# Kernel tuning notes

Measured on AMD Instinct MI355X. Metric: run time of the kernel, lower is better.

The kernel has to match this reference:

```python
import jax, jax.numpy as jnp
import numpy as np

N = 50000      # nodes
E = 1600000    # edges (before self loops)
IN = 128       # in_channels
HID = 64       # hidden_channels
HEADS = 2
NEG_SLOPE = 0.2  # PyG GATConv default


def setup_inputs() -> dict:
    key = jax.random.key(0)
    ks = jax.random.split(key, 12)
    s = 0.05
    return {
        "x": jax.random.normal(ks[0], (N, IN), jnp.float32),
        "edge_index": jax.random.randint(ks[1], (2, E), 0, N, dtype=jnp.int32),
        # layer 1: GATConv(IN -> HID, heads=HEADS, concat=True)
        "W1": jax.random.normal(ks[2], (IN, HEADS * HID), jnp.float32) * s,
        "a_src1": jax.random.normal(ks[3], (HEADS, HID), jnp.float32) * s,
        "a_dst1": jax.random.normal(ks[4], (HEADS, HID), jnp.float32) * s,
        "b1": jax.random.normal(ks[5], (HEADS * HID,), jnp.float32) * s,
        # layer 2: GATConv(HEADS*HID -> HID, heads=1, concat=False)
        "W2": jax.random.normal(ks[6], (HEADS * HID, HID), jnp.float32) * s,
        "a_src2": jax.random.normal(ks[7], (1, HID), jnp.float32) * s,
        "a_dst2": jax.random.normal(ks[8], (1, HID), jnp.float32) * s,
        "b2": jax.random.normal(ks[9], (HID,), jnp.float32) * s,
        "lin_w": jax.random.normal(ks[10], (HID, 1), jnp.float32) * s,
        "lin_b": jax.random.normal(ks[11], (1,), jnp.float32) * s,
    }


def gat_layer(x, src, dst, W, a_src, a_dst, b, heads, out_ch, concat, n):
    # linear transform: [n, heads, out_ch]
    h = (x @ W).reshape(n, heads, out_ch)
    # per-node attention logit halves  [n, heads]
    al_src = jnp.sum(h * a_src, axis=-1)
    al_dst = jnp.sum(h * a_dst, axis=-1)
    # per-edge logits (gather) + LeakyReLU  [e, heads]
    e = jax.nn.leaky_relu(al_src[src] + al_dst[dst], negative_slope=NEG_SLOPE)
    # segment softmax over edges grouped by destination node
    m = jax.ops.segment_max(e, dst, num_segments=n)
    ex = jnp.exp(e - m[dst])
    denom = jax.ops.segment_sum(ex, dst, num_segments=n)
    alpha = ex / (denom[dst] + 1e-16)
    # weighted message scatter-add  [n, heads, out_ch]
    out = jax.ops.segment_sum(h[src] * alpha[:, :, None], dst, num_segments=n)
    out = out.reshape(n, heads * out_ch) if concat else out.mean(axis=1)
    return out + b


def reference(x, edge_index, W1, a_src1, a_dst1, b1, W2, a_src2, a_dst2, b2, lin_w, lin_b):
    # PyG GATConv adds self loops by default
    loops = jnp.arange(N, dtype=edge_index.dtype)
    src = jnp.concatenate([edge_index[0], loops])
    dst = jnp.concatenate([edge_index[1], loops])
    h = gat_layer(x, src, dst, W1, a_src1, a_dst1, b1, HEADS, HID, True, N)
    h = jax.nn.elu(h)
    h = gat_layer(h, src, dst, W2, a_src2, a_dst2, b2, 1, HID, False, N)
    return (h @ lin_w + lin_b)[:, 0]  # squeeze(-1) -> [N]
```

## Files before the change

kernel.cpp:

```cpp
#include <hip/hip_runtime.h>
#include <hip/hip_fp16.h>


#define LEAKY(x) ((x) > 0.f ? (x) : 0.2f * (x))

typedef float v2f __attribute__((ext_vector_type(2)));
typedef _Float16 f16x8 __attribute__((ext_vector_type(8)));
typedef __fp16 h16x2 __attribute__((ext_vector_type(2)));
typedef float f32x4 __attribute__((ext_vector_type(4)));


template <int VPT>
__global__ __launch_bounds__(256) void bucket_cnt_kernel(const int* __restrict__ ei, int E, int n,
                                                         int* __restrict__ bc) {
  __shared__ int lc[256];
  int t = threadIdx.x;
  lc[t] = 0;
  __syncthreads();
  int base = blockIdx.x * (256 * VPT) + t;
  int tot = E + n;
#pragma unroll
  for (int u = 0; u < VPT; ++u) {
    int i = base + u * 256;
    if (i < tot) {
      int d = (i < E) ? ei[E + i] : (i - E);
      atomicAdd(&lc[d >> 8], 1);
    }
  }
  __syncthreads();
  if (lc[t]) atomicAdd(&bc[t], lc[t]);
}

template <int VPT>
__global__ __launch_bounds__(256) void bucket_scatter_kernel(const int* __restrict__ ei, int E,
                                                             int n,
                                                             const int* __restrict__ bcnt,
                                                             int* __restrict__ bcur_rel,
                                                             unsigned* __restrict__ entries,
                                                             int B) {
  __shared__ int lc[256];
  __shared__ int lbase[256];
  __shared__ int bscan[256];
  int t = threadIdx.x;
  lc[t] = 0;
  int v = (t < B) ? bcnt[t] : 0;
  bscan[t] = v;
  __syncthreads();
  for (int s = 1; s < 256; s <<= 1) {
    int a = (t >= s) ? bscan[t - s] : 0;
    __syncthreads();
    bscan[t] += a;
    __syncthreads();
  }
  int excl = bscan[t] - v;

  int base = blockIdx.x * (256 * VPT) + t;
  int tot = E + n;
  int bb[VPT], ll[VPT];
  unsigned pk[VPT];
#pragma unroll
  for (int u = 0; u < VPT; ++u) {
    int i = base + u * 256;
    bb[u] = -1;
    if (i < tot) {
      int s, d;
      if (i < E) { s = ei[i]; d = ei[E + i]; }
      else       { s = d = i - E; }
      int b = d >> 8;
      bb[u] = b;
      ll[u] = atomicAdd(&lc[b], 1);
      pk[u] = (unsigned)s | ((unsigned)(d & 255) << 16);
    }
  }
  __syncthreads();
  if (lc[t]) lbase[t] = excl + atomicAdd(&bcur_rel[t], lc[t]);
  __syncthreads();
#pragma unroll
  for (int u = 0; u < VPT; ++u)
    if (bb[u] >= 0) entries[lbase[bb[u]] + ll[u]] = pk[u];
}

__global__ __launch_bounds__(256) void csr_build_kernel(const unsigned* __restrict__ entries,
                                                        const int* __restrict__ bcnt,
                                                        int* __restrict__ off,
                                                        unsigned short* __restrict__ eps,
                                                        int n, int B) {
  __shared__ int bscan[256];
  __shared__ int hist[256];
  __shared__ int scn[256];
  __shared__ int cur[256];
  int b = blockIdx.x, t = threadIdx.x;
  int v = (t < B) ? bcnt[t] : 0;
  bscan[t] = v;
  __syncthreads();
  for (int s = 1; s < 256; s <<= 1) {
    int a = (t >= s) ? bscan[t - s] : 0;
    __syncthreads();
    bscan[t] += a;
    __syncthreads();
  }
  int k0 = (b == 0) ? 0 : bscan[b - 1];
  int k1 = bscan[b];
  __syncthreads();

  hist[t] = 0;
  __syncthreads();
  for (int k = k0 + t; k < k1; k += 256) atomicAdd(&hist[(entries[k] >> 16) & 255], 1);
  __syncthreads();
  int hv = hist[t];
  scn[t] = hv;
  __syncthreads();
  for (int s = 1; s < 256; s <<= 1) {
    int a = (t >= s) ? scn[t - s] : 0;
    __syncthreads();
    scn[t] += a;
    __syncthreads();
  }
  int excl = scn[t] - hv;
  int d = (b << 8) + t;
  if (d < n) off[d] = k0 + excl;
  cur[t] = k0 + excl;
  __syncthreads();
  for (int k = k0 + t; k < k1; k += 256) {
    unsigned e = entries[k];
    unsigned dl = (e >> 16) & 255;
    int p = atomicAdd(&cur[dl], 1);
    eps[p] = (unsigned short)(e & 0xffffu);
  }
}


__global__ __launch_bounds__(256) void wprep_kernel(const float* __restrict__ W1,
                                                    const float* __restrict__ W2,
                                                    const float* __restrict__ as2,
                                                    const float* __restrict__ ad2,
                                                    const float* __restrict__ lw,
                                                    unsigned short* __restrict__ Wp1,
                                                    float* __restrict__ vsrc2,
                                                    float* __restrict__ vdst2,
                                                    float* __restrict__ vlin,
                                                    int* __restrict__ bcnt,
                                                    int* __restrict__ bcur_rel,
                                                    int* __restrict__ off,
                                                    int B, int n, int Etot) {
  if (blockIdx.x == 0) {
    if (threadIdx.x <= (unsigned)B) {
      bcnt[threadIdx.x] = 0;
      bcur_rel[threadIdx.x] = 0;
    }
    if (threadIdx.x == 255) off[n] = Etot;
  }
  int t = blockIdx.x * 256 + threadIdx.x;
  if (t < 16384) {
    int e = t;
    int i = e & 7;
    int c = (e >> 3) & 15;
    int g = (e >> 7) & 3;
    int kk = (e >> 9) & 3;
    int cn = e >> 11;
    int k = kk * 32 + g * 8 + i;
    int col = cn * 16 + c;
    __half h = __float2half(W1[k * 128 + col]);
    Wp1[e] = *(unsigned short*)&h;
  } else if (t < 16384 + 128) {
    int k = t - 16384;
    float a = 0.f, b = 0.f, s = 0.f;
    for (int cc = 0; cc < 64; ++cc) {
      float w = W2[k * 64 + cc];
      a = fmaf(w, as2[cc], a);
      b = fmaf(w, ad2[cc], b);
      s = fmaf(w, lw[cc], s);
    }
    vsrc2[k] = a;
    vdst2[k] = b;
    vlin[k] = s;
  }
}


__global__ __launch_bounds__(256) void gemm1_kernel(const float* __restrict__ X,
                                                    const uint4* __restrict__ Wp,
                                                    const float* __restrict__ a_src,
                                                    const float* __restrict__ a_dst,
                                                    unsigned char* __restrict__ Hout,
                                                    float2* __restrict__ als,
                                                    float2* __restrict__ ald, int n) {
  __shared__ float Xl[32 * 132];
  __shared__ float lgt[2][2][2][16];
  int t = threadIdx.x;
  int wave = t >> 6, lane = t & 63;
  int wm = wave >> 1, wn = wave & 1;
  int g = lane >> 4, c = lane & 15;
  int nb0 = blockIdx.x * 32;

  {
    const float4* Xg = (const float4*)X;
    float4* Xs = (float4*)Xl;
#pragma unroll
    for (int u = 0; u < 4; ++u) {
      int idx = u * 256 + t;
      int r = idx >> 5, c4 = idx & 31;
      int row = nb0 + r;
      int rc = row < n ? row : (n - 1);
      Xs[r * 33 + c4] = Xg[(size_t)rc * 32 + c4];
    }
  }
  __syncthreads();

  f16x8 af[4];
  const float* xr = Xl + (wm * 16 + c) * 132 + g * 8;
#pragma unroll
  for (int kk = 0; kk < 4; ++kk) {
    float4 x0 = *(const float4*)(xr + kk * 32);
    float4 x1 = *(const float4*)(xr + kk * 32 + 4);
    union { f16x8 v; h16x2 p[4]; } A;
    A.p[0] = __builtin_amdgcn_cvt_pkrtz(x0.x, x0.y);
    A.p[1] = __builtin_amdgcn_cvt_pkrtz(x0.z, x0.w);
    A.p[2] = __builtin_amdgcn_cvt_pkrtz(x1.x, x1.y);
    A.p[3] = __builtin_amdgcn_cvt_pkrtz(x1.z, x1.w);
    af[kk] = A.v;
  }

  f32x4 acc[4];
  f32x4 z = {0.f, 0.f, 0.f, 0.f};
#pragma unroll
  for (int cn = 0; cn < 4; ++cn) acc[cn] = z;
#pragma unroll
  for (int cn = 0; cn < 4; ++cn) {
    int cng = wn * 4 + cn;
#pragma unroll
    for (int kk = 0; kk < 4; ++kk) {
      union { uint4 u; f16x8 v; } B;
      B.u = Wp[(cng * 4 + kk) * 64 + lane];
      acc[cn] = __builtin_amdgcn_mfma_f32_16x16x32_f16(af[kk], B.v, acc[cn], 0, 0, 0);
    }
  }

  float asv[4], adv[4];
#pragma unroll
  for (int cn = 0; cn < 4; ++cn) {
    int col_l = wn * 64 + cn * 16 + c;
    asv[cn] = a_src[col_l];
    adv[cn] = a_dst[col_l];
  }
  float ps[4] = {0.f, 0.f, 0.f, 0.f};
  float pd[4] = {0.f, 0.f, 0.f, 0.f};
#pragma unroll
  for (int cn = 0; cn < 4; ++cn) {
#pragma unroll
    for (int r = 0; r < 4; ++r) {
      float v = acc[cn][r];
      ps[r] = fmaf(v, asv[cn], ps[r]);
      pd[r] = fmaf(v, adv[cn], pd[r]);
      int noder = nb0 + wm * 16 + g * 4 + r;
      int colg = wn * 64 + cn * 16 + c;
      if (noder < n) {
        int b8 = __builtin_amdgcn_cvt_pk_fp8_f32(v, v, 0, false);
        Hout[(size_t)noder * 128 + colg] = (unsigned char)(b8 & 0xff);
      }
    }
  }
#pragma unroll
  for (int r = 0; r < 4; ++r) {
#pragma unroll
    for (int m = 1; m <= 8; m <<= 1) {
      ps[r] += __shfl_xor(ps[r], m, 64);
      pd[r] += __shfl_xor(pd[r], m, 64);
    }
  }
  if (c == 0) {
#pragma unroll
    for (int r = 0; r < 4; ++r) {
      lgt[wm][wn][0][g * 4 + r] = ps[r];
      lgt[wm][wn][1][g * 4 + r] = pd[r];
    }
  }
  __syncthreads();
  if (t < 32) {
    int wmm = t >> 4, row = t & 15;
    int node = nb0 + wmm * 16 + row;
    if (node < n) {
      als[node] = make_float2(lgt[wmm][0][0][row], lgt[wmm][1][0][row]);
      ald[node] = make_float2(lgt[wmm][0][1][row], lgt[wmm][1][1][row]);
    }
  }
}


__global__ __launch_bounds__(256) void agg1_kernel(const unsigned char* __restrict__ Hb8,
                                                   const float2* __restrict__ als,
                                                   const float2* __restrict__ ald,
                                                   const unsigned short* __restrict__ eps,
                                                   const int* __restrict__ off,
                                                   const float* __restrict__ b1,
                                                   const float* __restrict__ vsrc2,
                                                   const float* __restrict__ vdst2,
                                                   const float* __restrict__ vlin,
                                                   float2* __restrict__ gsrc,
                                                   float* __restrict__ adst2, int n) {
  __shared__ float wlds[4][128];
  int wid = (blockIdx.x * 256 + threadIdx.x) >> 6;
  int lane = threadIdx.x & 63;
  if (wid >= n) return;
  wid = __builtin_amdgcn_readfirstlane(wid);
  int wslot = (threadIdx.x >> 6) & 3;
  int half = lane >> 5;
  int k0 = off[wid], k1 = off[wid + 1];
  const unsigned short* Hu = (const unsigned short*)Hb8;
  float2 advv = ald[wid];
  float* wrow = &wlds[wslot][half << 6];

  float ax = 0.f, ay = 0.f, den = 0.f;

  for (int kb = k0; kb < k1; kb += 64) {
    int rem = min(k1 - kb, 64);
    int e = kb + (lane < rem ? lane : rem - 1);
    unsigned pp = eps[e];
    float2 l = als[pp];
    float g0 = __expf(LEAKY(l.x + advv.x));
    float g1 = __expf(LEAKY(l.y + advv.y));
    wlds[wslot][lane] = g0;
    wlds[wslot][64 + lane] = g1;

#define EDGE1(jj)                                                                   \
  {                                                                                 \
    unsigned p = (unsigned)__builtin_amdgcn_readlane((int)pp, (jj));                \
    float w = wrow[(jj)];                                                           \
    unsigned short hv = Hu[(p << 6) | (unsigned)lane];                              \
    v2f hf = __builtin_amdgcn_cvt_pk_f32_fp8((int)hv, false);                       \
    den += w;                                                                       \
    ax = fmaf(hf.x, w, ax);                                                         \
    ay = fmaf(hf.y, w, ay);                                                         \
  }

    int nb = rem >> 3;
    for (int b = 0; b < nb; ++b) {
      int jb = b << 3;
#pragma unroll
      for (int j = 0; j < 8; ++j) EDGE1(jb + j);
    }
    for (int jj = nb << 3; jj < rem; ++jj) EDGE1(jj);
#undef EDGE1
  }

  float inv = 1.f / (den + 1e-16f);
  float2 bv = ((const float2*)b1)[lane];
  float r0 = ax * inv + bv.x;
  float r1 = ay * inv + bv.y;
  r0 = r0 > 0.f ? r0 : (__expf(r0) - 1.f);
  r1 = r1 > 0.f ? r1 : (__expf(r1) - 1.f);
  float2 vs = ((const float2*)vsrc2)[lane];
  float2 vd = ((const float2*)vdst2)[lane];
  float2 vl = ((const float2*)vlin)[lane];
  float ps = r0 * vs.x + r1 * vs.y;
  float pd = r0 * vd.x + r1 * vd.y;
  float sv = r0 * vl.x + r1 * vl.y;
#pragma unroll
  for (int m = 1; m <= 32; m <<= 1) {
    ps += __shfl_xor(ps, m, 64);
    pd += __shfl_xor(pd, m, 64);
    sv += __shfl_xor(sv, m, 64);
  }
  if (lane == 0) {
    gsrc[wid] = make_float2(ps, sv);
    adst2[wid] = pd;
  }
}

__global__ __launch_bounds__(256) void agg2_kernel(const float2* __restrict__ gsrc,
                                                   const float* __restrict__ adst2,
                                                   const unsigned short* __restrict__ eps,
                                                   const int* __restrict__ off,
                                                   const float* __restrict__ b2,
                                                   const float* __restrict__ lin_w,
                                                   const float* __restrict__ lin_b,
                                                   float* __restrict__ out, int n) {
  int wid = (blockIdx.x * 256 + threadIdx.x) >> 6;
  int lane = threadIdx.x & 63;
  if (wid >= n) return;
  wid = __builtin_amdgcn_readfirstlane(wid);
  int k0 = off[wid], k1 = off[wid + 1];
  float adv = adst2[wid];

  float num = 0.f, den = 0.f;
  for (int kb = k0; kb < k1; kb += 64) {
    int e = kb + lane;
    bool ok = e < k1;
    unsigned pp = eps[ok ? e : k0];
    float2 g = gsrc[pp];
    float w = ok ? __expf(LEAKY(g.x + adv)) : 0.f;
    num = fmaf(w, g.y, num);
    den += w;
  }
  float bt = b2[lane] * lin_w[lane];
#pragma unroll
  for (int m = 1; m <= 32; m <<= 1) {
    num += __shfl_xor(num, m, 64);
    den += __shfl_xor(den, m, 64);
    bt  += __shfl_xor(bt, m, 64);
  }
  if (lane == 0) out[wid] = num / (den + 1e-16f) + bt + lin_b[0];
}


static inline size_t alignup(size_t v) { return (v + 255) & ~(size_t)255; }

extern "C" void kernel_launch(void* const* d_in, const int* in_sizes, int n_in,
                              void* d_out, int out_size, void* d_ws, size_t ws_size,
                              hipStream_t stream) {
  const float* x   = (const float*)d_in[0];
  const int*   ei  = (const int*)d_in[1];
  const float* W1  = (const float*)d_in[2];
  const float* as1 = (const float*)d_in[3];
  const float* ad1 = (const float*)d_in[4];
  const float* b1  = (const float*)d_in[5];
  const float* W2  = (const float*)d_in[6];
  const float* as2 = (const float*)d_in[7];
  const float* ad2 = (const float*)d_in[8];
  const float* b2  = (const float*)d_in[9];
  const float* lw  = (const float*)d_in[10];
  const float* lb  = (const float*)d_in[11];
  float* out = (float*)d_out;

  const int N = out_size;
  const int E = in_sizes[1] / 2;
  const int Etot = E + N;
  const int B = (N + 255) >> 8;

  char* p = (char*)d_ws;
  int* bcnt = (int*)p;  p += alignup((size_t)(B + 1) * 4);
  int* bcur_rel = (int*)p; p += alignup((size_t)(B + 1) * 4);
  unsigned* entries = (unsigned*)p; p += alignup((size_t)Etot * 4);
  int* off  = (int*)p;  p += alignup((size_t)(N + 1) * 4);
  unsigned short* eps = (unsigned short*)p; p += alignup((size_t)Etot * 2);
  float2* als = (float2*)p; p += alignup((size_t)N * 8);
  float2* ald = (float2*)p; p += alignup((size_t)N * 8);
  float2* gsrc = (float2*)p; p += alignup((size_t)N * 8);
  float* adst2 = (float*)p; p += alignup((size_t)N * 4);
  unsigned char* h1b = (unsigned char*)p; p += alignup((size_t)N * 128);
  unsigned short* wp1 = (unsigned short*)p; p += alignup((size_t)16384 * 2);
  float* vsrc2 = (float*)p; p += alignup((size_t)128 * 4);
  float* vdst2 = (float*)p; p += alignup((size_t)128 * 4);
  float* vlin  = (float*)p; p += alignup((size_t)128 * 4);

  constexpr int VPT = 8;
  int egrid = (Etot + 256 * VPT - 1) / (256 * VPT);

  wprep_kernel<<<65, 256, 0, stream>>>(W1, W2, as2, ad2, lw, wp1, vsrc2, vdst2, vlin,
                                       bcnt, bcur_rel, off, B, N, Etot);
  bucket_cnt_kernel<VPT><<<egrid, 256, 0, stream>>>(ei, E, N, bcnt);
  bucket_scatter_kernel<VPT><<<egrid, 256, 0, stream>>>(ei, E, N, bcnt, bcur_rel,
                                                        entries, B);
  csr_build_kernel<<<B, 256, 0, stream>>>(entries, bcnt, off, eps, N, B);

  gemm1_kernel<<<(N + 31) / 32, 256, 0, stream>>>(
      x, (const uint4*)wp1, as1, ad1, h1b, als, ald, N);
  agg1_kernel<<<(N + 3) / 4, 256, 0, stream>>>(h1b, als, ald, eps, off, b1,
                                               vsrc2, vdst2, vlin, gsrc, adst2, N);
  agg2_kernel<<<(N + 3) / 4, 256, 0, stream>>>(gsrc, adst2, eps, off, b2, lw, lb, out, N);
}
```

Measured before the change: 145.9 us.

## Merge weight prep with bucket count and GEMM with bucket scatter launches

Independent stages are now horizontally fused into shared launches: the weight preparation runs in the same grid as the bucket counting, and the layer-1 GEMM blocks share a grid with the bucket scatter blocks. Zeroing moves into its own tiny kernel, and the CSR build kernel goes from 256 to 512 threads per block. The aim is fewer launch gaps and letting the compute-bound GEMM overlap the atomic-heavy scatter. The cost is an extra launch and larger shared-memory use per combined block, which may lower occupancy.

```diff
diff --git a/kernel.cpp b/kernel.cpp
--- a/kernel.cpp
+++ b/kernel.cpp
@@ -10,14 +10,63 @@
 typedef float f32x4 __attribute__((ext_vector_type(4)));
 
 
+__global__ __launch_bounds__(256) void zero_kernel(int* __restrict__ bcnt,
+                                                   int* __restrict__ bcur_rel,
+                                                   int* __restrict__ off,
+                                                   int B, int n, int Etot) {
+  if (threadIdx.x <= (unsigned)B) {
+    bcnt[threadIdx.x] = 0;
+    bcur_rel[threadIdx.x] = 0;
+  }
+  if (threadIdx.x == 255) off[n] = Etot;
+}
+
+
 template <int VPT>
-__global__ __launch_bounds__(256) void bucket_cnt_kernel(const int* __restrict__ ei, int E, int n,
-                                                         int* __restrict__ bc) {
+__global__ __launch_bounds__(256) void prep_cnt_kernel(const float* __restrict__ W1,
+                                                       const float* __restrict__ W2,
+                                                       const float* __restrict__ as2,
+                                                       const float* __restrict__ ad2,
+                                                       const float* __restrict__ lw,
+                                                       unsigned short* __restrict__ Wp1,
+                                                       float* __restrict__ vsrc2,
+                                                       float* __restrict__ vdst2,
+                                                       float* __restrict__ vlin,
+                                                       const int* __restrict__ ei, int E, int n,
+                                                       int* __restrict__ bc, int WB) {
+  if ((int)blockIdx.x < WB) {
+    int t = blockIdx.x * 256 + threadIdx.x;
+    if (t < 16384) {
+      int e = t;
+      int i = e & 7;
+      int c = (e >> 3) & 15;
+      int g = (e >> 7) & 3;
+      int kk = (e >> 9) & 3;
+      int cn = e >> 11;
+      int k = kk * 32 + g * 8 + i;
+      int col = cn * 16 + c;
+      __half h = __float2half(W1[k * 128 + col]);
+      Wp1[e] = *(unsigned short*)&h;
+    } else if (t < 16384 + 128) {
+      int k = t - 16384;
+      float a = 0.f, b = 0.f, s = 0.f;
+      for (int cc = 0; cc < 64; ++cc) {
+        float w = W2[k * 64 + cc];
+        a = fmaf(w, as2[cc], a);
+        b = fmaf(w, ad2[cc], b);
+        s = fmaf(w, lw[cc], s);
+      }
+      vsrc2[k] = a;
+      vdst2[k] = b;
+      vlin[k] = s;
+    }
+    return;
+  }
   __shared__ int lc[256];
   int t = threadIdx.x;
   lc[t] = 0;
   __syncthreads();
-  int base = blockIdx.x * (256 * VPT) + t;
+  int base = (blockIdx.x - WB) * (256 * VPT) + t;
   int tot = E + n;
 #pragma unroll
   for (int u = 0; u < VPT; ++u) {
@@ -31,13 +80,117 @@
   if (lc[t]) atomicAdd(&bc[t], lc[t]);
 }
 
+
 template <int VPT>
-__global__ __launch_bounds__(256) void bucket_scatter_kernel(const int* __restrict__ ei, int E,
-                                                             int n,
-                                                             const int* __restrict__ bcnt,
-                                                             int* __restrict__ bcur_rel,
-                                                             unsigned* __restrict__ entries,
-                                                             int B) {
+__global__ __launch_bounds__(256) void gemm_scatter_kernel(
+    const float* __restrict__ X, const uint4* __restrict__ Wp,
+    const float* __restrict__ a_src, const float* __restrict__ a_dst,
+    unsigned char* __restrict__ Hout, float2* __restrict__ als, float2* __restrict__ ald,
+    const int* __restrict__ ei, int E, int n,
+    const int* __restrict__ bcnt, int* __restrict__ bcur_rel,
+    unsigned* __restrict__ entries, int B, int GB) {
+  if ((int)blockIdx.x < GB) {
+    __shared__ float Xl[32 * 132];
+    __shared__ float lgt[2][2][2][16];
+    int t = threadIdx.x;
+    int wave = t >> 6, lane = t & 63;
+    int wm = wave >> 1, wn = wave & 1;
+    int g = lane >> 4, c = lane & 15;
+    int nb0 = blockIdx.x * 32;
+
+    {
+      const float4* Xg = (const float4*)X;
+      float4* Xs = (float4*)Xl;
+#pragma unroll
+      for (int u = 0; u < 4; ++u) {
+        int idx = u * 256 + t;
+        int r = idx >> 5, c4 = idx & 31;
+        int row = nb0 + r;
+        int rc = row < n ? row : (n - 1);
+        Xs[r * 33 + c4] = Xg[(size_t)rc * 32 + c4];
+      }
+    }
+    __syncthreads();
+
+    f16x8 af[4];
+    const float* xr = Xl + (wm * 16 + c) * 132 + g * 8;
+#pragma unroll
+    for (int kk = 0; kk < 4; ++kk) {
+      float4 x0 = *(const float4*)(xr + kk * 32);
+      float4 x1 = *(const float4*)(xr + kk * 32 + 4);
+      union { f16x8 v; h16x2 p[4]; } A;
+      A.p[0] = __builtin_amdgcn_cvt_pkrtz(x0.x, x0.y);
+      A.p[1] = __builtin_amdgcn_cvt_pkrtz(x0.z, x0.w);
+      A.p[2] = __builtin_amdgcn_cvt_pkrtz(x1.x, x1.y);
+      A.p[3] = __builtin_amdgcn_cvt_pkrtz(x1.z, x1.w);
+      af[kk] = A.v;
+    }
+
+    f32x4 acc[4];
+    f32x4 z = {0.f, 0.f, 0.f, 0.f};
+#pragma unroll
+    for (int cn = 0; cn < 4; ++cn) acc[cn] = z;
+#pragma unroll
+    for (int cn = 0; cn < 4; ++cn) {
+      int cng = wn * 4 + cn;
+#pragma unroll
+      for (int kk = 0; kk < 4; ++kk) {
+        union { uint4 u; f16x8 v; } Bf;
+        Bf.u = Wp[(cng * 4 + kk) * 64 + lane];
+        acc[cn] = __builtin_amdgcn_mfma_f32_16x16x32_f16(af[kk], Bf.v, acc[cn], 0, 0, 0);
+      }
+    }
+
+    float asv[4], adv[4];
+#pragma unroll
+    for (int cn = 0; cn < 4; ++cn) {
+      int col_l = wn * 64 + cn * 16 + c;
+      asv[cn] = a_src[col_l];
+      adv[cn] = a_dst[col_l];
+    }
+    float ps[4] = {0.f, 0.f, 0.f, 0.f};
+    float pd[4] = {0.f, 0.f, 0.f, 0.f};
+#pragma unroll
+    for (int cn = 0; cn < 4; ++cn) {
+#pragma unroll
+      for (int r = 0; r < 4; ++r) {
+        float v = acc[cn][r];
+        ps[r] = fmaf(v, asv[cn], ps[r]);
+        pd[r] = fmaf(v, adv[cn], pd[r]);
+        int noder = nb0 + wm * 16 + g * 4 + r;
+        int colg = wn * 64 + cn * 16 + c;
+        if (noder < n) {
+          int b8 = __builtin_amdgcn_cvt_pk_fp8_f32(v, v, 0, false);
+          Hout[(size_t)noder * 128 + colg] = (unsigned char)(b8 & 0xff);
+        }
+      }
+    }
+#pragma unroll
+    for (int r = 0; r < 4; ++r) {
+#pragma unroll
+      for (int m = 1; m <= 8; m <<= 1) {
+        ps[r] += __shfl_xor(ps[r], m, 64);
+        pd[r] += __shfl_xor(pd[r], m, 64);
+      }
+    }
+    if (c == 0) {
+#pragma unroll
+      for (int r = 0; r < 4; ++r) {
+        lgt[wm][wn][0][g * 4 + r] = ps[r];
+        lgt[wm][wn][1][g * 4 + r] = pd[r];
+      }
+    }
+    __syncthreads();
+    if (t < 32) {
+      int wmm = t >> 4, row = t & 15;
+      int node = nb0 + wmm * 16 + row;
+      if (node < n) {
+        als[node] = make_float2(lgt[wmm][0][0][row], lgt[wmm][1][0][row]);
+        ald[node] = make_float2(lgt[wmm][0][1][row], lgt[wmm][1][1][row]);
+      }
+    }
+    return;
+  }
   __shared__ int lc[256];
   __shared__ int lbase[256];
   __shared__ int bscan[256];
@@ -54,7 +207,7 @@
   }
   int excl = bscan[t] - v;
 
-  int base = blockIdx.x * (256 * VPT) + t;
+  int base = (blockIdx.x - GB) * (256 * VPT) + t;
   int tot = E + n;
   int bb[VPT], ll[VPT];
   unsigned pk[VPT];
@@ -80,7 +233,8 @@
     if (bb[u] >= 0) entries[lbase[bb[u]] + ll[u]] = pk[u];
 }
 
-__global__ __launch_bounds__(256) void csr_build_kernel(const unsigned* __restrict__ entries,
+
+__global__ __launch_bounds__(512) void csr_build_kernel(const unsigned* __restrict__ entries,
                                                         const int* __restrict__ bcnt,
                                                         int* __restrict__ off,
                                                         unsigned short* __restrict__ eps,
@@ -90,199 +244,42 @@
   __shared__ int scn[256];
   __shared__ int cur[256];
   int b = blockIdx.x, t = threadIdx.x;
-  int v = (t < B) ? bcnt[t] : 0;
-  bscan[t] = v;
+  if (t < 256) bscan[t] = (t < B) ? bcnt[t] : 0;
   __syncthreads();
   for (int s = 1; s < 256; s <<= 1) {
-    int a = (t >= s) ? bscan[t - s] : 0;
-    __syncthreads();
-    bscan[t] += a;
+    int a = (t >= (unsigned)s && t < 256) ? bscan[t - s] : 0;
+    __syncthreads();
+    if (t < 256) bscan[t] += a;
     __syncthreads();
   }
   int k0 = (b == 0) ? 0 : bscan[b - 1];
   int k1 = bscan[b];
-  __syncthreads();
-
-  hist[t] = 0;
-  __syncthreads();
-  for (int k = k0 + t; k < k1; k += 256) atomicAdd(&hist[(entries[k] >> 16) & 255], 1);
-  __syncthreads();
-  int hv = hist[t];
-  scn[t] = hv;
+
+  if (t < 256) hist[t] = 0;
+  __syncthreads();
+  for (int k = k0 + t; k < k1; k += 512) atomicAdd(&hist[(entries[k] >> 16) & 255], 1);
+  __syncthreads();
+  int hv = (t < 256) ? hist[t] : 0;
+  if (t < 256) scn[t] = hv;
   __syncthreads();
   for (int s = 1; s < 256; s <<= 1) {
-    int a = (t >= s) ? scn[t - s] : 0;
-    __syncthreads();
-    scn[t] += a;
-    __syncthreads();
-  }
-  int excl = scn[t] - hv;
-  int d = (b << 8) + t;
-  if (d < n) off[d] = k0 + excl;
-  cur[t] = k0 + excl;
-  __syncthreads();
-  for (int k = k0 + t; k < k1; k += 256) {
+    int a = (t >= (unsigned)s && t < 256) ? scn[t - s] : 0;
+    __syncthreads();
+    if (t < 256) scn[t] += a;
+    __syncthreads();
+  }
+  if (t < 256) {
+    int excl = scn[t] - hv;
+    int d = (b << 8) + t;
+    if (d < n) off[d] = k0 + excl;
+    cur[t] = k0 + excl;
+  }
+  __syncthreads();
+  for (int k = k0 + t; k < k1; k += 512) {
     unsigned e = entries[k];
     unsigned dl = (e >> 16) & 255;
     int p = atomicAdd(&cur[dl], 1);
     eps[p] = (unsigned short)(e & 0xffffu);
-  }
-}
-
-
-__global__ __launch_bounds__(256) void wprep_kernel(const float* __restrict__ W1,
-                                                    const float* __restrict__ W2,
-                                                    const float* __restrict__ as2,
-                                                    const float* __restrict__ ad2,
-                                                    const float* __restrict__ lw,
-                                                    unsigned short* __restrict__ Wp1,
-                                                    float* __restrict__ vsrc2,
-                                                    float* __restrict__ vdst2,
-                                                    float* __restrict__ vlin,
-                                                    int* __restrict__ bcnt,
-                                                    int* __restrict__ bcur_rel,
-                                                    int* __restrict__ off,
-                                                    int B, int n, int Etot) {
-  if (blockIdx.x == 0) {
-    if (threadIdx.x <= (unsigned)B) {
-      bcnt[threadIdx.x] = 0;
-      bcur_rel[threadIdx.x] = 0;
-    }
-    if (threadIdx.x == 255) off[n] = Etot;
-  }
-  int t = blockIdx.x * 256 + threadIdx.x;
-  if (t < 16384) {
-    int e = t;
-    int i = e & 7;
-    int c = (e >> 3) & 15;
-    int g = (e >> 7) & 3;
-    int kk = (e >> 9) & 3;
-    int cn = e >> 11;
-    int k = kk * 32 + g * 8 + i;
-    int col = cn * 16 + c;
-    __half h = __float2half(W1[k * 128 + col]);
-    Wp1[e] = *(unsigned short*)&h;
-  } else if (t < 16384 + 128) {
-    int k = t - 16384;
-    float a = 0.f, b = 0.f, s = 0.f;
-    for (int cc = 0; cc < 64; ++cc) {
-      float w = W2[k * 64 + cc];
-      a = fmaf(w, as2[cc], a);
-      b = fmaf(w, ad2[cc], b);
-      s = fmaf(w, lw[cc], s);
-    }
-    vsrc2[k] = a;
-    vdst2[k] = b;
-    vlin[k] = s;
-  }
-}
-
-
-__global__ __launch_bounds__(256) void gemm1_kernel(const float* __restrict__ X,
-                                                    const uint4* __restrict__ Wp,
-                                                    const float* __restrict__ a_src,
-                                                    const float* __restrict__ a_dst,
-                                                    unsigned char* __restrict__ Hout,
-                                                    float2* __restrict__ als,
-                                                    float2* __restrict__ ald, int n) {
-  __shared__ float Xl[32 * 132];
-  __shared__ float lgt[2][2][2][16];
-  int t = threadIdx.x;
-  int wave = t >> 6, lane = t & 63;
-  int wm = wave >> 1, wn = wave & 1;
-  int g = lane >> 4, c = lane & 15;
-  int nb0 = blockIdx.x * 32;
-
-  {
-    const float4* Xg = (const float4*)X;
-    float4* Xs = (float4*)Xl;
-#pragma unroll
-    for (int u = 0; u < 4; ++u) {
-      int idx = u * 256 + t;
-      int r = idx >> 5, c4 = idx & 31;
-      int row = nb0 + r;
-      int rc = row < n ? row : (n - 1);
-      Xs[r * 33 + c4] = Xg[(size_t)rc * 32 + c4];
-    }
-  }
-  __syncthreads();
-
-  f16x8 af[4];
-  const float* xr = Xl + (wm * 16 + c) * 132 + g * 8;
-#pragma unroll
-  for (int kk = 0; kk < 4; ++kk) {
-    float4 x0 = *(const float4*)(xr + kk * 32);
-    float4 x1 = *(const float4*)(xr + kk * 32 + 4);
-    union { f16x8 v; h16x2 p[4]; } A;
-    A.p[0] = __builtin_amdgcn_cvt_pkrtz(x0.x, x0.y);
-    A.p[1] = __builtin_amdgcn_cvt_pkrtz(x0.z, x0.w);
-    A.p[2] = __builtin_amdgcn_cvt_pkrtz(x1.x, x1.y);
-    A.p[3] = __builtin_amdgcn_cvt_pkrtz(x1.z, x1.w);
-    af[kk] = A.v;
-  }
-
-  f32x4 acc[4];
-  f32x4 z = {0.f, 0.f, 0.f, 0.f};
-#pragma unroll
-  for (int cn = 0; cn < 4; ++cn) acc[cn] = z;
-#pragma unroll
-  for (int cn = 0; cn < 4; ++cn) {
-    int cng = wn * 4 + cn;
-#pragma unroll
-    for (int kk = 0; kk < 4; ++kk) {
-      union { uint4 u; f16x8 v; } B;
-      B.u = Wp[(cng * 4 + kk) * 64 + lane];
-      acc[cn] = __builtin_amdgcn_mfma_f32_16x16x32_f16(af[kk], B.v, acc[cn], 0, 0, 0);
-    }
-  }
-
-  float asv[4], adv[4];
-#pragma unroll
-  for (int cn = 0; cn < 4; ++cn) {
-    int col_l = wn * 64 + cn * 16 + c;
-    asv[cn] = a_src[col_l];
-    adv[cn] = a_dst[col_l];
-  }
-  float ps[4] = {0.f, 0.f, 0.f, 0.f};
-  float pd[4] = {0.f, 0.f, 0.f, 0.f};
-#pragma unroll
-  for (int cn = 0; cn < 4; ++cn) {
-#pragma unroll
-    for (int r = 0; r < 4; ++r) {
-      float v = acc[cn][r];
-      ps[r] = fmaf(v, asv[cn], ps[r]);
-      pd[r] = fmaf(v, adv[cn], pd[r]);
-      int noder = nb0 + wm * 16 + g * 4 + r;
-      int colg = wn * 64 + cn * 16 + c;
-      if (noder < n) {
-        int b8 = __builtin_amdgcn_cvt_pk_fp8_f32(v, v, 0, false);
-        Hout[(size_t)noder * 128 + colg] = (unsigned char)(b8 & 0xff);
-      }
-    }
-  }
-#pragma unroll
-  for (int r = 0; r < 4; ++r) {
-#pragma unroll
-    for (int m = 1; m <= 8; m <<= 1) {
-      ps[r] += __shfl_xor(ps[r], m, 64);
-      pd[r] += __shfl_xor(pd[r], m, 64);
-    }
-  }
-  if (c == 0) {
-#pragma unroll
-    for (int r = 0; r < 4; ++r) {
-      lgt[wm][wn][0][g * 4 + r] = ps[r];
-      lgt[wm][wn][1][g * 4 + r] = pd[r];
-    }
-  }
-  __syncthreads();
-  if (t < 32) {
-    int wmm = t >> 4, row = t & 15;
-    int node = nb0 + wmm * 16 + row;
-    if (node < n) {
-      als[node] = make_float2(lgt[wmm][0][0][row], lgt[wmm][1][0][row]);
-      ald[node] = make_float2(lgt[wmm][0][1][row], lgt[wmm][1][1][row]);
-    }
   }
 }
 
@@ -367,6 +364,7 @@
   }
 }
 
+
 __global__ __launch_bounds__(256) void agg2_kernel(const float2* __restrict__ gsrc,
                                                    const float* __restrict__ adst2,
                                                    const unsigned short* __restrict__ eps,
@@ -445,16 +443,17 @@
 
   constexpr int VPT = 8;
   int egrid = (Etot + 256 * VPT - 1) / (256 * VPT);
-
-  wprep_kernel<<<65, 256, 0, stream>>>(W1, W2, as2, ad2, lw, wp1, vsrc2, vdst2, vlin,
-                                       bcnt, bcur_rel, off, B, N, Etot);
-  bucket_cnt_kernel<VPT><<<egrid, 256, 0, stream>>>(ei, E, N, bcnt);
-  bucket_scatter_kernel<VPT><<<egrid, 256, 0, stream>>>(ei, E, N, bcnt, bcur_rel,
-                                                        entries, B);
-  csr_build_kernel<<<B, 256, 0, stream>>>(entries, bcnt, off, eps, N, B);
-
-  gemm1_kernel<<<(N + 31) / 32, 256, 0, stream>>>(
-      x, (const uint4*)wp1, as1, ad1, h1b, als, ald, N);
+  constexpr int WB = 65;
+  int GB = (N + 31) / 32;
+
+  zero_kernel<<<1, 256, 0, stream>>>(bcnt, bcur_rel, off, B, N, Etot);
+  prep_cnt_kernel<VPT><<<WB + egrid, 256, 0, stream>>>(
+      W1, W2, as2, ad2, lw, wp1, vsrc2, vdst2, vlin, ei, E, N, bcnt, WB);
+  gemm_scatter_kernel<VPT><<<GB + egrid, 256, 0, stream>>>(
+      x, (const uint4*)wp1, as1, ad1, h1b, als, ald,
+      ei, E, N, bcnt, bcur_rel, entries, B, GB);
+  csr_build_kernel<<<B, 512, 0, stream>>>(entries, bcnt, off, eps, N, B);
+
   agg1_kernel<<<(N + 3) / 4, 256, 0, stream>>>(h1b, als, ald, eps, off, b1,
                                                vsrc2, vdst2, vlin, gsrc, adst2, N);
   agg2_kernel<<<(N + 3) / 4, 256, 0, stream>>>(gsrc, adst2, eps, off, b2, lw, lb, out, N);
```

Result: faster. 133.2 us (-8.8%).
